# Kernel optimization log

Measured on AMD Instinct MI355X. Metric: run time of the kernel, lower is better.

The kernel has to match this reference:

```python
import jax, jax.numpy as jnp
import numpy as np

C, K, H = 256, 64, 1024


def squash(t):
    # t: [C, H]; norm = sum of squares over last dim (matches torch code)
    norm = jnp.sum(t * t, axis=-1, keepdims=True)  # [C, 1]
    scale = norm / (1.0 + norm)
    return scale * t / jnp.sqrt(norm)


def setup_inputs() -> dict:
    key = jax.random.key(0)
    k1, k2 = jax.random.split(key)
    encoder_output = jax.random.normal(k1, (C, K, H), dtype=jnp.float32)
    # nn.Linear weight [out, in]; scaled init for numerical sanity
    W = jax.random.normal(k2, (H, H), dtype=jnp.float32) * (1.0 / np.sqrt(H))
    return {"encoder_output": encoder_output, "W": W, "iter_routing": 3}


def reference(encoder_output, W, iter_routing):
    # encoder_output: [C, K, H], W: [H, H] (l_1 weight, no bias)
    # The linear projection is loop-invariant in the original; hoist it.
    x_hat = jnp.einsum('ckh,dh->ckd', encoder_output, W)  # [C, K, H]
    b = jnp.zeros(encoder_output.shape[:2], dtype=encoder_output.dtype)  # [C, K]
    c = None
    for _ in range(iter_routing):
        d = jax.nn.softmax(b, axis=-1)                       # [C, K]
        c_hat = jnp.sum(x_hat * d[..., None], axis=1)        # [C, H]
        c = squash(c_hat)                                    # [C, H]
        b = b + jnp.einsum('ckh,ch->ck', x_hat, c)           # [C, K]
    return c
```

## Files before the change

### kernel.cpp

```cpp
#include <hip/hip_runtime.h>


using f32x4  = __attribute__((ext_vector_type(4))) float;
using f32x2  = __attribute__((ext_vector_type(2))) float;
using bf16x8 = __attribute__((ext_vector_type(8))) __bf16;
using bf16x4 = __attribute__((ext_vector_type(4))) __bf16;

struct BfPair { __bf16 hi, lo; };
__device__ inline BfPair split_bf16(float x) {
    BfPair p;
    p.hi = (__bf16)x;
    p.lo = (__bf16)(x - (float)p.hi);
    return p;
}

#define PIN_ER16(er) asm volatile("" : \
    "+v"(er[0][0]), "+v"(er[0][1]), "+v"(er[0][2]), "+v"(er[0][3]), \
    "+v"(er[1][0]), "+v"(er[1][1]), "+v"(er[1][2]), "+v"(er[1][3]), \
    "+v"(er[2][0]), "+v"(er[2][1]), "+v"(er[2][2]), "+v"(er[2][3]), \
    "+v"(er[3][0]), "+v"(er[3][1]), "+v"(er[3][2]), "+v"(er[3][3]))

struct RoutSM {
    float spart[16][1024];
    float u_s[1024];
    float b_s[64], d_s[64], red_s[16], scale_s;
};

template <int MODE>
__device__ __forceinline__ void routing_body(
    int c, const float* __restrict__ enc, const float* __restrict__ y0,
    const float* __restrict__ y1, float* __restrict__ bglob,
    __bf16* __restrict__ s_hi, __bf16* __restrict__ s_lo, RoutSM* sm)
{
    const int t = threadIdx.x, lane = t & 63, w = t >> 6;
    const float* E = enc + (size_t)c * 65536;

    float yv = 0.f, sv = 0.f;
    if (MODE > 0) {
        const size_t o = (size_t)c * 1024 + t;
        yv = y0[o] + y1[o];
        sv = (float)s_hi[o] + (float)s_lo[o];
    }

    f32x4 er[4][4];
    #pragma unroll
    for (int r = 0; r < 4; ++r) {
        const float* ek = E + (size_t)(w * 4 + r) * 1024 + lane * 8;
        er[r][0] = *(const f32x4*)(ek);
        er[r][1] = *(const f32x4*)(ek + 4);
        er[r][2] = *(const f32x4*)(ek + 512);
        er[r][3] = *(const f32x4*)(ek + 516);
    }
    PIN_ER16(er);

    if (MODE > 0) {
        sm->u_s[t] = yv;
        float p = yv * sv;
        #pragma unroll
        for (int off = 32; off; off >>= 1) p += __shfl_xor(p, off, 64);
        if (lane == 0) sm->red_s[w] = p;
        __syncthreads();
        if (t == 0) {
            float n = 0.f;
            #pragma unroll
            for (int i = 0; i < 16; ++i) n += sm->red_s[i];
            sm->scale_s = n / ((1.f + n) * sqrtf(n) + 1e-30f);
        }
        __syncthreads();
        const float scale = sm->scale_s;
        f32x4 uf[4];
        uf[0] = *(const f32x4*)&sm->u_s[lane * 8];
        uf[1] = *(const f32x4*)&sm->u_s[lane * 8 + 4];
        uf[2] = *(const f32x4*)&sm->u_s[512 + lane * 8];
        uf[3] = *(const f32x4*)&sm->u_s[512 + lane * 8 + 4];
        #pragma unroll
        for (int r = 0; r < 4; ++r) {
            float sum = 0.f;
            #pragma unroll
            for (int q = 0; q < 4; ++q)
                #pragma unroll
                for (int j = 0; j < 4; ++j)
                    sum += er[r][q][j] * uf[q][j];
            #pragma unroll
            for (int off = 32; off; off >>= 1) sum += __shfl_xor(sum, off, 64);
            if (lane == 0) {
                const int k = w * 4 + r;
                const float bv =
                    (MODE == 2 ? bglob[c * 64 + k] : 0.f) + scale * sum;
                bglob[c * 64 + k] = bv;
                sm->b_s[k] = bv;
            }
        }
    }
    __syncthreads();

    if (MODE == 0) {
        if (t < 64) sm->d_s[t] = 1.f / 64.f;
    } else if (t < 64) {
        float bv = sm->b_s[t], m = bv;
        #pragma unroll
        for (int off = 32; off; off >>= 1) m = fmaxf(m, __shfl_xor(m, off, 64));
        const float e = expf(bv - m);
        float smm = e;
        #pragma unroll
        for (int off = 32; off; off >>= 1) smm += __shfl_xor(smm, off, 64);
        sm->d_s[t] = e / smm;
    }
    __syncthreads();

    PIN_ER16(er);

    #pragma unroll
    for (int q = 0; q < 4; ++q) {
        f32x4 p = {};
        #pragma unroll
        for (int r = 0; r < 4; ++r) {
            const float dk = sm->d_s[w * 4 + r];
            #pragma unroll
            for (int j = 0; j < 4; ++j) p[j] += dk * er[r][q][j];
        }
        const int h = (q >> 1) * 512 + lane * 8 + (q & 1) * 4;
        *(f32x4*)&sm->spart[w][h] = p;
    }
    __syncthreads();

    {
        float a = 0.f;
        #pragma unroll
        for (int wv = 0; wv < 16; ++wv) a += sm->spart[wv][t];
        const BfPair p = split_bf16(a);
        s_hi[(size_t)c * 1024 + t] = p.hi;
        s_lo[(size_t)c * 1024 + t] = p.lo;
    }
}

template <int MODE, int WITH_CONV>
__global__ __launch_bounds__(1024, 4)
__attribute__((amdgpu_waves_per_eu(4, 4)))
void routing_kernel(
    const float* __restrict__ enc, const float* __restrict__ y0,
    const float* __restrict__ y1, float* __restrict__ bglob,
    __bf16* __restrict__ s_hi, __bf16* __restrict__ s_lo,
    const float* __restrict__ W, __bf16* __restrict__ Wt_hi,
    __bf16* __restrict__ Wt_lo)
{
    __shared__ union {
        RoutSM r;
        float tile[64][65];
    } sm;

    int c = blockIdx.x;
    if (WITH_CONV) {
        if (blockIdx.x < 256) {
            const int by = blockIdx.x >> 4, bx = blockIdx.x & 15;
            const int tx = threadIdx.x & 63, ty = threadIdx.x >> 6;
            for (int i = ty; i < 64; i += 16)
                sm.tile[i][tx] = W[(size_t)(by * 64 + i) * 1024 + bx * 64 + tx];
            __syncthreads();
            for (int i = ty; i < 64; i += 16) {
                const size_t idx = (size_t)(bx * 64 + i) * 1024 + by * 64 + tx;
                const BfPair p = split_bf16(sm.tile[tx][i]);
                Wt_hi[idx] = p.hi;
                Wt_lo[idx] = p.lo;
            }
            return;
        }
        c = blockIdx.x - 256;
    }
    routing_body<MODE>(c, enc, y0, y1, bglob, s_hi, s_lo, &sm.r);
}

struct QSmem {
    __bf16 a_hi[64 * 64];
    __bf16 a_lo[64 * 64];
    __bf16 b_hi[64 * 64];
    __bf16 b_lo[64 * 64];
};

__device__ __forceinline__ int swz128(int row, int colbyte) {
    return row * 128 + (colbyte ^ ((row & 7) << 4));
}

__global__ __launch_bounds__(256) void gemm_q_kernel(
    const __bf16* __restrict__ Wt_hi, const __bf16* __restrict__ Wt_lo,
    __bf16* __restrict__ Q_hi, __bf16* __restrict__ Q_lo)
{
    __shared__ QSmem sm;
    const int b = blockIdx.x;
    int tj = (int)((sqrtf(8.f * (float)b + 1.f) - 1.f) * 0.5f);
    while ((tj + 1) * (tj + 2) / 2 <= b) ++tj;
    while (tj * (tj + 1) / 2 > b) --tj;
    const int ti = b - tj * (tj + 1) / 2;

    const int t = threadIdx.x;
    const int lane = t & 63, w = t >> 6;
    const int wr = w >> 1, wc = w & 1;
    const int sr  = t >> 2;
    const int scb = (t & 3) * 16;
    const size_t ga = (size_t)(ti * 64 + sr) * 1024 + scb / 2;
    const size_t gb = (size_t)(tj * 64 + sr) * 1024 + scb / 2;

    f32x4 acc[2][2] = {};
    for (int k0 = 0; k0 < 1024; k0 += 64) {
        if (k0) __syncthreads();
        #pragma unroll
        for (int h = 0; h < 2; ++h) {
            const int cb = scb + h * 64;
            const size_t gao = ga + h * 32 + k0;
            const size_t gbo = gb + h * 32 + k0;
            *(bf16x8*)((char*)sm.a_hi + swz128(sr, cb)) = *(const bf16x8*)(Wt_hi + gao);
            *(bf16x8*)((char*)sm.a_lo + swz128(sr, cb)) = *(const bf16x8*)(Wt_lo + gao);
            *(bf16x8*)((char*)sm.b_hi + swz128(sr, cb)) = *(const bf16x8*)(Wt_hi + gbo);
            *(bf16x8*)((char*)sm.b_lo + swz128(sr, cb)) = *(const bf16x8*)(Wt_lo + gbo);
        }
        __syncthreads();
        #pragma unroll
        for (int kk = 0; kk < 2; ++kk) {
            const int cb = kk * 64 + (lane >> 4) * 16;
            bf16x8 ah[2], al[2], bh[2], bl[2];
            #pragma unroll
            for (int mi = 0; mi < 2; ++mi) {
                const int m = wr * 32 + mi * 16 + (lane & 15);
                ah[mi] = *(const bf16x8*)((char*)sm.a_hi + swz128(m, cb));
                al[mi] = *(const bf16x8*)((char*)sm.a_lo + swz128(m, cb));
            }
            #pragma unroll
            for (int ni = 0; ni < 2; ++ni) {
                const int n = wc * 32 + ni * 16 + (lane & 15);
                bh[ni] = *(const bf16x8*)((char*)sm.b_hi + swz128(n, cb));
                bl[ni] = *(const bf16x8*)((char*)sm.b_lo + swz128(n, cb));
            }
            #pragma unroll
            for (int mi = 0; mi < 2; ++mi)
                #pragma unroll
                for (int ni = 0; ni < 2; ++ni) {
                    f32x4 a = acc[mi][ni];
                    a = __builtin_amdgcn_mfma_f32_16x16x32_bf16(ah[mi], bh[ni], a, 0, 0, 0);
                    a = __builtin_amdgcn_mfma_f32_16x16x32_bf16(ah[mi], bl[ni], a, 0, 0, 0);
                    a = __builtin_amdgcn_mfma_f32_16x16x32_bf16(al[mi], bh[ni], a, 0, 0, 0);
                    acc[mi][ni] = a;
                }
        }
    }
    const int rr = (lane >> 4) * 4, colb = lane & 15;
    #pragma unroll
    for (int mi = 0; mi < 2; ++mi)
        #pragma unroll
        for (int ni = 0; ni < 2; ++ni) {
            bf16x4 hv, lv;
            #pragma unroll
            for (int r = 0; r < 4; ++r) {
                const BfPair p = split_bf16(acc[mi][ni][r]);
                const size_t idx =
                    (size_t)(ti * 64 + wr * 32 + mi * 16 + rr + r) * 1024 +
                    tj * 64 + wc * 32 + ni * 16 + colb;
                Q_hi[idx] = p.hi;
                Q_lo[idx] = p.lo;
                hv[r] = p.hi;
                lv[r] = p.lo;
            }
            if (ti != tj) {
                const size_t midx =
                    (size_t)(tj * 64 + wc * 32 + ni * 16 + colb) * 1024 +
                    ti * 64 + wr * 32 + mi * 16 + rr;
                *(bf16x4*)(Q_hi + midx) = hv;
                *(bf16x4*)(Q_lo + midx) = lv;
            }
        }
}

template <int CONV>
__global__ __launch_bounds__(256) void gemm_nt_kernel(
    const __bf16* __restrict__ Ah, const __bf16* __restrict__ Al,
    const __bf16* __restrict__ Bh, const __bf16* __restrict__ Bl,
    float* __restrict__ C0, float* __restrict__ C1,
    const float* __restrict__ Wsrc, __bf16* __restrict__ Wd_hi,
    __bf16* __restrict__ Wd_lo)
{
    __shared__ QSmem sm;
    if (CONV && blockIdx.x >= 128) {
        const int b = blockIdx.x - 128;
        const size_t base = (size_t)b * 4096 + (threadIdx.x << 2);
        #pragma unroll
        for (int q = 0; q < 4; ++q) {
            const size_t idx = base + (size_t)q * 1024;
            const f32x4 v = *(const f32x4*)(Wsrc + idx);
            bf16x4 hv, lv;
            #pragma unroll
            for (int j = 0; j < 4; ++j) {
                const BfPair p = split_bf16(v[j]);
                hv[j] = p.hi;
                lv[j] = p.lo;
            }
            *(bf16x4*)(Wd_hi + idx) = hv;
            *(bf16x4*)(Wd_lo + idx) = lv;
        }
        return;
    }

    const int kh   = blockIdx.x & 1;
    const int task = blockIdx.x >> 1;
    const int mt   = task >> 4;
    const int nt   = task & 15;
    const int t = threadIdx.x;
    const int lane = t & 63, w = t >> 6;
    const int wr = w >> 1, wc = w & 1;
    const int sr  = t >> 2;
    const int scb = (t & 3) * 16;
    const size_t ga = (size_t)(mt * 64 + sr) * 1024 + kh * 512 + scb / 2;
    const size_t gb = (size_t)(nt * 64 + sr) * 1024 + kh * 512 + scb / 2;

    f32x4 acc[2][2] = {};
    for (int k0 = 0; k0 < 512; k0 += 64) {
        if (k0) __syncthreads();
        #pragma unroll
        for (int h = 0; h < 2; ++h) {
            const int cb = scb + h * 64;
            const size_t gao = ga + h * 32 + k0;
            const size_t gbo = gb + h * 32 + k0;
            *(bf16x8*)((char*)sm.a_hi + swz128(sr, cb)) = *(const bf16x8*)(Ah + gao);
            *(bf16x8*)((char*)sm.a_lo + swz128(sr, cb)) = *(const bf16x8*)(Al + gao);
            *(bf16x8*)((char*)sm.b_hi + swz128(sr, cb)) = *(const bf16x8*)(Bh + gbo);
            *(bf16x8*)((char*)sm.b_lo + swz128(sr, cb)) = *(const bf16x8*)(Bl + gbo);
        }
        __syncthreads();
        #pragma unroll
        for (int kk = 0; kk < 2; ++kk) {
            const int cb = kk * 64 + (lane >> 4) * 16;
            bf16x8 ah[2], al[2], bh[2], bl[2];
            #pragma unroll
            for (int mi = 0; mi < 2; ++mi) {
                const int m = wr * 32 + mi * 16 + (lane & 15);
                ah[mi] = *(const bf16x8*)((char*)sm.a_hi + swz128(m, cb));
                al[mi] = *(const bf16x8*)((char*)sm.a_lo + swz128(m, cb));
            }
            #pragma unroll
            for (int ni = 0; ni < 2; ++ni) {
                const int n = wc * 32 + ni * 16 + (lane & 15);
                bh[ni] = *(const bf16x8*)((char*)sm.b_hi + swz128(n, cb));
                bl[ni] = *(const bf16x8*)((char*)sm.b_lo + swz128(n, cb));
            }
            #pragma unroll
            for (int mi = 0; mi < 2; ++mi)
                #pragma unroll
                for (int ni = 0; ni < 2; ++ni) {
                    f32x4 a = acc[mi][ni];
                    a = __builtin_amdgcn_mfma_f32_16x16x32_bf16(ah[mi], bh[ni], a, 0, 0, 0);
                    a = __builtin_amdgcn_mfma_f32_16x16x32_bf16(ah[mi], bl[ni], a, 0, 0, 0);
                    a = __builtin_amdgcn_mfma_f32_16x16x32_bf16(al[mi], bh[ni], a, 0, 0, 0);
                    acc[mi][ni] = a;
                }
        }
    }
    float* Cc = kh ? C1 : C0;
    const int rr = (lane >> 4) * 4, colb = lane & 15;
    #pragma unroll
    for (int mi = 0; mi < 2; ++mi)
        #pragma unroll
        for (int ni = 0; ni < 2; ++ni)
            #pragma unroll
            for (int r = 0; r < 4; ++r)
                Cc[(size_t)(mt * 64 + wr * 32 + mi * 16 + rr + r) * 1024 +
                   nt * 64 + wc * 32 + ni * 16 + colb] = acc[mi][ni][r];
}

__global__ __launch_bounds__(256) void squash_out_kernel(
    const float* __restrict__ chat0, const float* __restrict__ chat1,
    float* __restrict__ outp)
{
    __shared__ float wsum[4];
    const int c = blockIdx.x, t = threadIdx.x;
    const int lane = t & 63, w = t >> 6;
    const size_t o = (size_t)c * 1024 + t * 4;
    f32x4 v = *(const f32x4*)(chat0 + o) + *(const f32x4*)(chat1 + o);
    float ss = v[0]*v[0] + v[1]*v[1] + v[2]*v[2] + v[3]*v[3];
    #pragma unroll
    for (int off = 32; off; off >>= 1) ss += __shfl_xor(ss, off, 64);
    if (lane == 0) wsum[w] = ss;
    __syncthreads();
    const float norm = wsum[0] + wsum[1] + wsum[2] + wsum[3];
    const float scale = norm / ((1.f + norm) * sqrtf(norm) + 1e-30f);
    *(f32x4*)(outp + o) = v * scale;
}

__global__ __launch_bounds__(512) void fallback_kernel(
    const float* __restrict__ enc, const float* __restrict__ W,
    float* __restrict__ outp)
{
    __shared__ float u_s[1024], s_s[1024], c_s[1024], chat_s[1024];
    __shared__ float b_s[64], d_s[64], red_s[8];
    const int t = threadIdx.x, lane = t & 63, w = t >> 6;
    const float* erow = enc + (size_t)blockIdx.x * 65536;

    if (t < 64) b_s[t] = 0.f;
    __syncthreads();

    for (int it = 0; it < 3; ++it) {
        if (it > 0) {
            f32x4 uf[4];
            #pragma unroll
            for (int q = 0; q < 2; ++q) {
                uf[2*q]   = *(const f32x4*)&u_s[q*512 + lane*8];
                uf[2*q+1] = *(const f32x4*)&u_s[q*512 + lane*8 + 4];
            }
            for (int r = 0; r < 8; ++r) {
                const int k = w * 8 + r;
                const float* ek = erow + (size_t)k * 1024;
                float sum = 0.f;
                #pragma unroll
                for (int q = 0; q < 2; ++q) {
                    f32x4 e0 = *(const f32x4*)(ek + q*512 + lane*8);
                    f32x4 e1 = *(const f32x4*)(ek + q*512 + lane*8 + 4);
                    #pragma unroll
                    for (int j = 0; j < 4; ++j) {
                        sum += e0[j] * uf[2*q][j];
                        sum += e1[j] * uf[2*q+1][j];
                    }
                }
                #pragma unroll
                for (int off = 32; off; off >>= 1) sum += __shfl_xor(sum, off, 64);
                if (lane == 0) b_s[k] += sum;
            }
            __syncthreads();
        }
        if (t < 64) {
            float bv = b_s[t], m = bv;
            #pragma unroll
            for (int off = 32; off; off >>= 1) m = fmaxf(m, __shfl_xor(m, off, 64));
            float e = expf(bv - m), sm = e;
            #pragma unroll
            for (int off = 32; off; off >>= 1) sm += __shfl_xor(sm, off, 64);
            d_s[t] = e / sm;
        }
        __syncthreads();
        {
            const int h0 = t * 2;
            float a0 = 0.f, a1 = 0.f;
            for (int k = 0; k < 64; ++k) {
                f32x2 ev = *(const f32x2*)(erow + (size_t)k * 1024 + h0);
                a0 += d_s[k] * ev[0]; a1 += d_s[k] * ev[1];
            }
            s_s[h0] = a0; s_s[h0+1] = a1;
        }
        __syncthreads();
        {
            f32x4 sf[4];
            #pragma unroll
            for (int q = 0; q < 2; ++q) {
                sf[2*q]   = *(const f32x4*)&s_s[q*512 + lane*8];
                sf[2*q+1] = *(const f32x4*)&s_s[q*512 + lane*8 + 4];
            }
            for (int r = 0; r < 128; ++r) {
                const int d = w * 128 + r;
                const float* wr = W + (size_t)d * 1024;
                float sum = 0.f;
                #pragma unroll
                for (int q = 0; q < 2; ++q) {
                    f32x4 w0 = *(const f32x4*)(wr + q*512 + lane*8);
                    f32x4 w1 = *(const f32x4*)(wr + q*512 + lane*8 + 4);
                    #pragma unroll
                    for (int j = 0; j < 4; ++j) {
                        sum += w0[j] * sf[2*q][j];
                        sum += w1[j] * sf[2*q+1][j];
                    }
                }
                #pragma unroll
                for (int off = 32; off; off >>= 1) sum += __shfl_xor(sum, off, 64);
                if (lane == 0) chat_s[d] = sum;
            }
        }
        __syncthreads();
        {
            const int h0 = t * 2;
            float v0 = chat_s[h0], v1 = chat_s[h0+1];
            float ss = v0*v0 + v1*v1;
            #pragma unroll
            for (int off = 32; off; off >>= 1) ss += __shfl_xor(ss, off, 64);
            if (lane == 0) red_s[w] = ss;
            __syncthreads();
            float norm = 0.f;
            #pragma unroll
            for (int i = 0; i < 8; ++i) norm += red_s[i];
            const float scale = norm / ((1.f + norm) * sqrtf(norm) + 1e-30f);
            c_s[h0] = v0 * scale; c_s[h0+1] = v1 * scale;
        }
        __syncthreads();
        if (it < 2) {
            const int h0 = t * 2;
            float uu0 = 0.f, uu1 = 0.f;
            for (int d = 0; d < 1024; ++d) {
                f32x2 wv = *(const f32x2*)(W + (size_t)d * 1024 + h0);
                uu0 += c_s[d] * wv[0]; uu1 += c_s[d] * wv[1];
            }
            u_s[h0] = uu0; u_s[h0+1] = uu1;
        } else {
            const int h0 = t * 2;
            f32x2 ov; ov[0] = c_s[h0]; ov[1] = c_s[h0+1];
            *(f32x2*)(outp + (size_t)blockIdx.x * 1024 + h0) = ov;
        }
        __syncthreads();
    }
}

extern "C" void kernel_launch(void* const* d_in, const int* in_sizes, int n_in,
                              void* d_out, int out_size, void* d_ws, size_t ws_size,
                              hipStream_t stream)
{
    const float* enc = (const float*)d_in[0];
    const float* W   = (const float*)d_in[1];
    float* outp = (float*)d_out;
    (void)in_sizes; (void)n_in; (void)out_size;

    char* ws = (char*)d_ws;
    float*  b     = (float*) (ws + 0x000000);
    __bf16* s_hi  = (__bf16*)(ws + 0x080000);
    __bf16* s_lo  = (__bf16*)(ws + 0x100000);
    float*  y0    = (float*) (ws + 0x180000);
    float*  y1    = (float*) (ws + 0x280000);
    __bf16* Wx_hi = (__bf16*)(ws + 0x380000);
    __bf16* Wx_lo = (__bf16*)(ws + 0x580000);
    __bf16* Q_hi  = (__bf16*)(ws + 0x780000);
    __bf16* Q_lo  = (__bf16*)(ws + 0x980000);

    if (ws_size < 0xB80000) {
        fallback_kernel<<<256, 512, 0, stream>>>(enc, W, outp);
        return;
    }

    routing_kernel<0, 1><<<512, 1024, 0, stream>>>(
        enc, y0, y1, b, s_hi, s_lo, W, Wx_hi, Wx_lo);

    gemm_q_kernel<<<136, 256, 0, stream>>>(Wx_hi, Wx_lo, Q_hi, Q_lo);

    gemm_nt_kernel<1><<<384, 256, 0, stream>>>(
        s_hi, s_lo, Q_hi, Q_lo, y0, y1, W, Wx_hi, Wx_lo);

    routing_kernel<1, 0><<<256, 1024, 0, stream>>>(
        enc, y0, y1, b, s_hi, s_lo, nullptr, nullptr, nullptr);

    gemm_nt_kernel<0><<<128, 256, 0, stream>>>(
        s_hi, s_lo, Q_hi, Q_lo, y0, y1, nullptr, nullptr, nullptr);

    routing_kernel<2, 0><<<256, 1024, 0, stream>>>(
        enc, y0, y1, b, s_hi, s_lo, nullptr, nullptr, nullptr);

    gemm_nt_kernel<0><<<128, 256, 0, stream>>>(
        s_hi, s_lo, Wx_hi, Wx_lo, y0, y1, nullptr, nullptr, nullptr);

    squash_out_kernel<<<256, 256, 0, stream>>>(y0, y1, outp);
}
```

Baseline: 188.3 us.

## Stream encoder slices through double-buffered LDS chunks with async global-to-LDS loads

The routing kernel no longer holds each capsule's 64x1024 encoder slice in registers. It streams the slice in eight 8-row chunks through a double-buffered LDS region using global_load_lds, with explicit vmcnt waits and barriers, and reads the slice twice (once for the b update, once for the weighted sum). This removes the large register footprint and the forced occupancy attributes, and overlaps global loads with compute. In exchange it doubles global or L2 traffic for the encoder in MODE>0 and adds many block-wide barriers per chunk.

After: 219.0 us. +16.3%, slower.

```diff
diff --git a/kernel.cpp b/kernel.cpp
--- a/kernel.cpp
+++ b/kernel.cpp
@@ -14,17 +14,49 @@
     return p;
 }
 
-#define PIN_ER16(er) asm volatile("" : \
-    "+v"(er[0][0]), "+v"(er[0][1]), "+v"(er[0][2]), "+v"(er[0][3]), \
-    "+v"(er[1][0]), "+v"(er[1][1]), "+v"(er[1][2]), "+v"(er[1][3]), \
-    "+v"(er[2][0]), "+v"(er[2][1]), "+v"(er[2][2]), "+v"(er[2][3]), \
-    "+v"(er[3][0]), "+v"(er[3][1]), "+v"(er[3][2]), "+v"(er[3][3]))
-
 struct RoutSM {
-    float spart[16][1024];
-    float u_s[1024];
-    float b_s[64], d_s[64], red_s[16], scale_s;
+    float chunk[2][8][1024];
+    float bpart[16][64];
+    float bold[64];
+    float d_s[64], red_s[16], scale_s;
 };
+struct QSmem {
+    __bf16 a_hi[64 * 64];
+    __bf16 a_lo[64 * 64];
+    __bf16 b_hi[64 * 64];
+    __bf16 b_lo[64 * 64];
+};
+
+typedef const __attribute__((address_space(1))) unsigned int* GASP;
+typedef __attribute__((address_space(3))) unsigned int* LASP;
+
+__device__ __forceinline__ void stage_chunk(
+    const float* __restrict__ E, float* __restrict__ chunkbase,
+    int t, int w, int ck, int cb)
+{
+    const float* s1 = E + (size_t)ck * 8192 + (size_t)t * 4;
+    float* d1 = chunkbase + cb * 8192 + w * 256;
+    __builtin_amdgcn_global_load_lds((GASP)s1, (LASP)d1, 16, 0, 0);
+    __builtin_amdgcn_global_load_lds((GASP)(s1 + 4096), (LASP)(d1 + 4096),
+                                     16, 0, 0);
+}
+
+#define CHUNK_READY(ck)                                                  \
+    do {                                                                 \
+        if ((ck) < 7) asm volatile("s_waitcnt vmcnt(2)" ::: "memory");   \
+        else          asm volatile("s_waitcnt vmcnt(0)" ::: "memory");   \
+        __builtin_amdgcn_sched_barrier(0);                               \
+        __builtin_amdgcn_s_barrier();                                    \
+        __builtin_amdgcn_sched_barrier(0);                               \
+    } while (0)
+
+#define CHUNK_FREE()                                                     \
+    do {                                                                 \
+        asm volatile("s_waitcnt lgkmcnt(0)" ::: "memory");               \
+        __builtin_amdgcn_sched_barrier(0);                               \
+        __builtin_amdgcn_s_barrier();                                    \
+        __builtin_amdgcn_sched_barrier(0);                               \
+    } while (0)
 
 template <int MODE>
 __device__ __forceinline__ void routing_body(
@@ -34,31 +66,18 @@
 {
     const int t = threadIdx.x, lane = t & 63, w = t >> 6;
     const float* E = enc + (size_t)c * 65536;
-
-    float yv = 0.f, sv = 0.f;
+    float* const cbase = &sm->chunk[0][0][0];
+
+    float yv = 0.f;
     if (MODE > 0) {
         const size_t o = (size_t)c * 1024 + t;
         yv = y0[o] + y1[o];
-        sv = (float)s_hi[o] + (float)s_lo[o];
-    }
-
-    f32x4 er[4][4];
-    #pragma unroll
-    for (int r = 0; r < 4; ++r) {
-        const float* ek = E + (size_t)(w * 4 + r) * 1024 + lane * 8;
-        er[r][0] = *(const f32x4*)(ek);
-        er[r][1] = *(const f32x4*)(ek + 4);
-        er[r][2] = *(const f32x4*)(ek + 512);
-        er[r][3] = *(const f32x4*)(ek + 516);
-    }
-    PIN_ER16(er);
-
-    if (MODE > 0) {
-        sm->u_s[t] = yv;
+        const float sv = (float)s_hi[o] + (float)s_lo[o];
         float p = yv * sv;
         #pragma unroll
         for (int off = 32; off; off >>= 1) p += __shfl_xor(p, off, 64);
         if (lane == 0) sm->red_s[w] = p;
+        if (t < 64) sm->bold[t] = (MODE == 2) ? bglob[c * 64 + t] : 0.f;
         __syncthreads();
         if (t == 0) {
             float n = 0.f;
@@ -66,78 +85,73 @@
             for (int i = 0; i < 16; ++i) n += sm->red_s[i];
             sm->scale_s = n / ((1.f + n) * sqrtf(n) + 1e-30f);
         }
-        __syncthreads();
-        const float scale = sm->scale_s;
-        f32x4 uf[4];
-        uf[0] = *(const f32x4*)&sm->u_s[lane * 8];
-        uf[1] = *(const f32x4*)&sm->u_s[lane * 8 + 4];
-        uf[2] = *(const f32x4*)&sm->u_s[512 + lane * 8];
-        uf[3] = *(const f32x4*)&sm->u_s[512 + lane * 8 + 4];
-        #pragma unroll
-        for (int r = 0; r < 4; ++r) {
+    }
+
+    stage_chunk(E, cbase, t, w, 0, 0);
+    stage_chunk(E, cbase, t, w, 1, 1);
+
+    if (MODE > 0) {
+        #pragma unroll
+        for (int ck = 0; ck < 8; ++ck) {
+            CHUNK_READY(ck);
+            const int cb = ck & 1;
+            #pragma unroll
+            for (int r = 0; r < 8; ++r) {
+                float p = sm->chunk[cb][r][t] * yv;
+                #pragma unroll
+                for (int off = 32; off; off >>= 1)
+                    p += __shfl_xor(p, off, 64);
+                if (lane == 0) sm->bpart[w][ck * 8 + r] = p;
+            }
+            CHUNK_FREE();
+            if (ck < 6) stage_chunk(E, cbase, t, w, ck + 2, cb);
+        }
+        if (t < 64) {
             float sum = 0.f;
             #pragma unroll
-            for (int q = 0; q < 4; ++q)
-                #pragma unroll
-                for (int j = 0; j < 4; ++j)
-                    sum += er[r][q][j] * uf[q][j];
-            #pragma unroll
-            for (int off = 32; off; off >>= 1) sum += __shfl_xor(sum, off, 64);
-            if (lane == 0) {
-                const int k = w * 4 + r;
-                const float bv =
-                    (MODE == 2 ? bglob[c * 64 + k] : 0.f) + scale * sum;
-                bglob[c * 64 + k] = bv;
-                sm->b_s[k] = bv;
-            }
-        }
-    }
-    __syncthreads();
-
-    if (MODE == 0) {
-        if (t < 64) sm->d_s[t] = 1.f / 64.f;
-    } else if (t < 64) {
-        float bv = sm->b_s[t], m = bv;
-        #pragma unroll
-        for (int off = 32; off; off >>= 1) m = fmaxf(m, __shfl_xor(m, off, 64));
-        const float e = expf(bv - m);
-        float smm = e;
-        #pragma unroll
-        for (int off = 32; off; off >>= 1) smm += __shfl_xor(smm, off, 64);
-        sm->d_s[t] = e / smm;
-    }
-    __syncthreads();
-
-    PIN_ER16(er);
-
+            for (int wv = 0; wv < 16; ++wv) sum += sm->bpart[wv][t];
+            const float bv = sm->bold[t] + sm->scale_s * sum;
+            bglob[c * 64 + t] = bv;
+            float m = bv;
+            #pragma unroll
+            for (int off = 32; off; off >>= 1)
+                m = fmaxf(m, __shfl_xor(m, off, 64));
+            const float e = expf(bv - m);
+            float smm = e;
+            #pragma unroll
+            for (int off = 32; off; off >>= 1)
+                smm += __shfl_xor(smm, off, 64);
+            sm->d_s[t] = e / smm;
+        }
+        stage_chunk(E, cbase, t, w, 0, 0);
+        stage_chunk(E, cbase, t, w, 1, 1);
+        asm volatile("s_waitcnt lgkmcnt(0)" ::: "memory");
+        __builtin_amdgcn_sched_barrier(0);
+        __builtin_amdgcn_s_barrier();
+        __builtin_amdgcn_sched_barrier(0);
+    }
+
+    float acc = 0.f;
     #pragma unroll
-    for (int q = 0; q < 4; ++q) {
-        f32x4 p = {};
-        #pragma unroll
-        for (int r = 0; r < 4; ++r) {
-            const float dk = sm->d_s[w * 4 + r];
-            #pragma unroll
-            for (int j = 0; j < 4; ++j) p[j] += dk * er[r][q][j];
-        }
-        const int h = (q >> 1) * 512 + lane * 8 + (q & 1) * 4;
-        *(f32x4*)&sm->spart[w][h] = p;
-    }
-    __syncthreads();
-
-    {
-        float a = 0.f;
-        #pragma unroll
-        for (int wv = 0; wv < 16; ++wv) a += sm->spart[wv][t];
-        const BfPair p = split_bf16(a);
-        s_hi[(size_t)c * 1024 + t] = p.hi;
-        s_lo[(size_t)c * 1024 + t] = p.lo;
-    }
+    for (int ck = 0; ck < 8; ++ck) {
+        CHUNK_READY(ck);
+        const int cb = ck & 1;
+        #pragma unroll
+        for (int r = 0; r < 8; ++r) {
+            const float dk = (MODE == 0) ? 0.015625f : sm->d_s[ck * 8 + r];
+            acc += dk * sm->chunk[cb][r][t];
+        }
+        CHUNK_FREE();
+        if (ck < 6) stage_chunk(E, cbase, t, w, ck + 2, cb);
+    }
+
+    const BfPair p = split_bf16(acc);
+    s_hi[(size_t)c * 1024 + t] = p.hi;
+    s_lo[(size_t)c * 1024 + t] = p.lo;
 }
 
 template <int MODE, int WITH_CONV>
-__global__ __launch_bounds__(1024, 4)
-__attribute__((amdgpu_waves_per_eu(4, 4)))
-void routing_kernel(
+__global__ __launch_bounds__(1024) void routing_kernel(
     const float* __restrict__ enc, const float* __restrict__ y0,
     const float* __restrict__ y1, float* __restrict__ bglob,
     __bf16* __restrict__ s_hi, __bf16* __restrict__ s_lo,
@@ -170,13 +184,6 @@
     routing_body<MODE>(c, enc, y0, y1, bglob, s_hi, s_lo, &sm.r);
 }
 
-struct QSmem {
-    __bf16 a_hi[64 * 64];
-    __bf16 a_lo[64 * 64];
-    __bf16 b_hi[64 * 64];
-    __bf16 b_lo[64 * 64];
-};
-
 __device__ __forceinline__ int swz128(int row, int colbyte) {
     return row * 128 + (colbyte ^ ((row & 7) << 4));
 }
```
